# Optimization experiments

Measured on AMD Instinct MI355X. Metric: run time of the kernel, lower is better.

The kernel has to match this reference:

```python
import jax, jax.numpy as jnp
import numpy as np

D_MODEL = 384
N_HEADS = 8
HEAD_DIM = D_MODEL // N_HEADS


def setup_inputs() -> dict:
    key = jax.random.key(0)
    ks = jax.random.split(key, 8)
    b, n = 2, 2048
    s = 0.02
    return {
        "x": jax.random.normal(ks[0], (b, n, D_MODEL), jnp.float32),
        "coords": jax.random.normal(ks[1], (b, n, 3), jnp.float32),
        "W_qkv": jax.random.normal(ks[2], (D_MODEL, 3 * D_MODEL), jnp.float32) * s,
        "b_qkv": jnp.zeros((3 * D_MODEL,), jnp.float32),
        "W_dist": jax.random.normal(ks[3], (1, N_HEADS), jnp.float32) * s,
        "b_dist": jnp.zeros((N_HEADS,), jnp.float32),
        "W_out": jax.random.normal(ks[4], (D_MODEL, D_MODEL), jnp.float32) * s,
        "b_out": jnp.zeros((D_MODEL,), jnp.float32),
    }


def reference(x, coords, W_qkv, b_qkv, W_dist, b_dist, W_out, b_out):
    b, n, _ = x.shape
    qkv = x @ W_qkv + b_qkv                       # (b, n, 3*d)
    q, k, v = jnp.split(qkv, 3, axis=-1)
    def heads(t):
        return t.reshape(b, n, N_HEADS, HEAD_DIM).transpose(0, 2, 1, 3)  # b h n d
    q, k, v = heads(q), heads(k), heads(v)
    attn = jnp.einsum('bhid,bhjd->bhij', q, k) / jnp.sqrt(jnp.float32(HEAD_DIM))
    # distance bias: ||c_i - c_j|| projected to heads (Linear(1, n_heads))
    diff = coords[:, :, None, :] - coords[:, None, :, :]   # (b, i, j, 3)
    dist = jnp.sqrt(jnp.sum(diff * diff, axis=-1))         # (b, i, j)
    dist_bias = dist[..., None] * W_dist[0] + b_dist       # (b, i, j, h)
    attn = attn + dist_bias.transpose(0, 3, 1, 2)          # (b, h, i, j)
    attn = jax.nn.softmax(attn, axis=-1)
    out = jnp.einsum('bhij,bhjd->bhid', attn, v)
    out = out.transpose(0, 2, 1, 3).reshape(b, n, D_MODEL)
    return out @ W_out + b_out
```

## Files before the change

### kernel.cpp

```cpp
#include <hip/hip_runtime.h>
#include <hip/hip_bf16.h>

#define NB 2
#define SEQ 2048
#define DM 384
#define NH 8
#define HD 48
#define QKVN 1152

typedef __hip_bfloat16 bf16;
typedef __attribute__((ext_vector_type(8))) short short8;
typedef __attribute__((ext_vector_type(4))) float float4v;
typedef __attribute__((ext_vector_type(16))) float f32x16;

static __device__ __forceinline__ float bf2f(bf16 v){ return __bfloat162float(v); }
static __device__ __forceinline__ float ldin(const void* p, size_t i, int isf){
    return isf ? ((const float*)p)[i] : bf2f(((const bf16*)p)[i]);
}
static __device__ __forceinline__ short f2b(float f){
    union { float f; unsigned u; } a; a.f = f;
    unsigned r = a.u + 0x7FFFu + ((a.u >> 16) & 1u);
    return (short)(r >> 16);
}
static __device__ __forceinline__ unsigned pk2(float a, float b){
    union { __hip_bfloat162 h; unsigned u; } r;
    r.h = __float22bfloat162_rn(float2{a, b});
    return r.u;
}
static __device__ __forceinline__ float bflo(unsigned u){
    union { unsigned u; float f; } a; a.u = u << 16; return a.f;
}
static __device__ __forceinline__ float bfhi(unsigned u){
    union { unsigned u; float f; } a; a.u = u & 0xFFFF0000u; return a.f;
}
static __device__ __forceinline__ short8 u4pack(unsigned w0, unsigned w1, unsigned w2, unsigned w3){
    union { unsigned u[4]; short8 s; } r; r.u[0]=w0; r.u[1]=w1; r.u[2]=w2; r.u[3]=w3; return r.s;
}
static __device__ __forceinline__ int detect_isf(const void* x){
    const unsigned short* xb = (const unsigned short*)x;
    int l = threadIdx.x & 63;
    union { unsigned u; float f; } a; a.u = ((unsigned)xb[2*l]) << 16;
    float ab = fabsf(a.f);
    int good = (a.f == 0.0f) || (ab > 9.765625e-4f && ab < 1024.0f);
    unsigned long long m = __ballot(good);
    return (__popcll(m) >= 32) ? 0 : 1;
}

__global__ __launch_bounds__(256) void k_wt(const void* __restrict__ x,
    const void* __restrict__ Wqkv, const void* __restrict__ Wout,
    const void* __restrict__ bqkv, const void* __restrict__ bout,
    const void* __restrict__ Wdist, const void* __restrict__ bdist,
    short* __restrict__ WqT, short* __restrict__ WoT,
    float* __restrict__ bqf, float* __restrict__ bof,
    float* __restrict__ wdf, float* __restrict__ bdf)
{
    const int isf = detect_isf(x);
    const int t = threadIdx.x;
    const int b = blockIdx.x;
    if (b < 576) {
        int bb, NW; const void* W; short* WT;
        if (b < 432) { bb = b;       NW = QKVN; W = Wqkv; WT = WqT; }
        else         { bb = b - 432; NW = DM;   W = Wout; WT = WoT; }
        int ntiles = NW >> 5;
        int kt = bb / ntiles, nt = bb % ntiles;
        int k0 = kt*32, n0 = nt*32;
        __shared__ float Ls[32][33];
        for (int idx = t; idx < 1024; idx += 256) {
            int r = idx >> 5, c = idx & 31;
            Ls[r][c] = ldin(W, (size_t)(k0+r)*NW + n0 + c, isf);
        }
        __syncthreads();
        for (int idx = t; idx < 1024; idx += 256) {
            int r2 = idx >> 5, c2 = idx & 31;
            WT[(size_t)(n0+r2)*DM + k0 + c2] = f2b(Ls[c2][r2]);
        }
    } else {
        int idx = (b - 576)*256 + t;
        const float log2e = 1.4426950408889634f;
        if (idx < QKVN) bqf[idx] = ldin(bqkv, idx, isf);
        else if (idx < QKVN + DM) bof[idx - QKVN] = ldin(bout, idx - QKVN, isf);
        else if (idx < QKVN + DM + NH) wdf[idx - QKVN - DM] = ldin(Wdist, idx - QKVN - DM, isf)*log2e;
        else if (idx < QKVN + DM + 2*NH) bdf[idx - QKVN - DM - NH] = ldin(bdist, idx - QKVN - DM - NH, isf)*log2e;
    }
}

__global__ __launch_bounds__(256) void k_qkv_dist(const void* __restrict__ x,
    const void* __restrict__ coords,
    const short* __restrict__ WT, const float* __restrict__ bias,
    short* __restrict__ qg3, short* __restrict__ kg3, short* __restrict__ vg3,
    short* __restrict__ dist8)
{
    __shared__ __align__(16) short As[64*72];
    __shared__ __align__(16) short Bs[128*72];
    __shared__ float cjx[16], cjy[16], cjz[16];
    const int isf = detect_isf(x);
    const int t = threadIdx.x;
    if (blockIdx.x >= 576) {
        const int b = blockIdx.x - 576;
        const int bb = b >> 8;
        const int jg = (b >> 1) & 127;
        const int j0 = jg * 16;
        const int ih = (b & 1) * 1024;
        if (t < 16) {
            int gj = (bb*SEQ + j0 + t)*3;
            cjx[t] = ldin(coords, gj, isf);
            cjy[t] = ldin(coords, gj+1, isf);
            cjz[t] = ldin(coords, gj+2, isf);
        }
        __syncthreads();
        #pragma unroll
        for (int k = 0; k < 4; ++k) {
            int i = ih + k*256 + t;
            int gi = (bb*SEQ + i)*3;
            float px = ldin(coords, gi, isf), py = ldin(coords, gi+1, isf), pz = ldin(coords, gi+2, isf);
            short o[16];
            #pragma unroll
            for (int e = 0; e < 16; ++e) {
                float dx = px - cjx[e], dy = py - cjy[e], dz = pz - cjz[e];
                o[e] = f2b(sqrtf(dx*dx + dy*dy + dz*dz));
            }
            short* dst = dist8 + (((size_t)bb*512 + (size_t)jg*4)*SEQ + i)*4;
            *(int2*)(dst)          = *(const int2*)(o);
            *(int2*)(dst + SEQ*4)  = *(const int2*)(o + 4);
            *(int2*)(dst + SEQ*8)  = *(const int2*)(o + 8);
            *(int2*)(dst + SEQ*12) = *(const int2*)(o + 12);
        }
        return;
    }
    const int w = t >> 6, lane = t & 63, L = lane & 15, quad = lane >> 4;
    const int mt = blockIdx.x / 9, nt = blockIdx.x % 9;
    const int row0 = mt*64, col0 = nt*128;
    const int wm = w & 1, wn = w >> 1;
    float4v acc[2][4] = {};
    for (int k0 = 0; k0 < DM; k0 += 64) {
        __syncthreads();
        for (int c = t; c < 512; c += 256) {
            int row = c >> 3, k8 = c & 7;
            size_t src = (size_t)(row0+row)*DM + k0 + k8*8;
            if (isf) {
                const float* xf = (const float*)x + src;
                short o[8];
                #pragma unroll
                for (int e = 0; e < 8; ++e) o[e] = f2b(xf[e]);
                *(int4*)(&As[row*72 + k8*8]) = *(const int4*)o;
            } else {
                *(int4*)(&As[row*72 + k8*8]) = *(const int4*)((const short*)x + src);
            }
        }
        for (int c = t; c < 1024; c += 256) {
            int row = c >> 3, k8 = c & 7;
            *(int4*)(&Bs[row*72 + k8*8]) = *(const int4*)(WT + (size_t)(col0+row)*DM + k0 + k8*8);
        }
        __syncthreads();
        #pragma unroll
        for (int kc = 0; kc < 2; ++kc) {
            short8 a0 = *(const short8*)(&As[(32*wm + L)*72 + kc*32 + quad*8]);
            short8 a1 = *(const short8*)(&As[(32*wm + 16 + L)*72 + kc*32 + quad*8]);
            #pragma unroll
            for (int ni = 0; ni < 4; ++ni) {
                short8 bf = *(const short8*)(&Bs[(64*wn + 16*ni + L)*72 + kc*32 + quad*8]);
                acc[0][ni] = __builtin_amdgcn_mfma_f32_16x16x32_bf16(a0, bf, acc[0][ni], 0, 0, 0);
                acc[1][ni] = __builtin_amdgcn_mfma_f32_16x16x32_bf16(a1, bf, acc[1][ni], 0, 0, 0);
            }
        }
    }
    const int which = col0 / DM;
    const int cbase = col0 % DM;
    short* Ep = Bs;
    __syncthreads();
    if (which < 2) {
        #pragma unroll
        for (int mi = 0; mi < 2; ++mi)
            #pragma unroll
            for (int ni = 0; ni < 4; ++ni) {
                int col_l = 64*wn + 16*ni + L;
                float bv = bias[col0 + col_l];
                #pragma unroll
                for (int r = 0; r < 4; ++r) {
                    int row_l = 32*wm + 16*mi + quad*4 + r;
                    Ep[row_l*136 + col_l] = f2b(acc[mi][ni][r] + bv);
                }
            }
        __syncthreads();
        short* dst = which ? kg3 : qg3;
        for (int c = t; c < 1024; c += 256) {
            int row_l = c >> 4, col_l = (c & 15)*8;
            int row_g = row0 + row_l;
            int bi = row_g >> 11, nn = row_g & (SEQ-1);
            int c2 = cbase + col_l;
            int hh = c2/HD, dh = c2%HD;
            int bh = bi*NH + hh;
            int dc = dh >> 4, hi = (dh >> 3) & 1;
            size_t dstoff = ((size_t)bh*64 + (nn>>5))*1536 + (size_t)((dc*2 + hi)*256 + (nn&31)*8);
            *(int4*)(dst + dstoff) = *(const int4*)(&Ep[row_l*136 + col_l]);
        }
    } else {
        #pragma unroll
        for (int mi = 0; mi < 2; ++mi)
            #pragma unroll
            for (int ni = 0; ni < 4; ++ni) {
                int col_l = 64*wn + 16*ni + L;
                float bv = bias[col0 + col_l];
                #pragma unroll
                for (int r = 0; r < 4; ++r) {
                    int row_l = 32*wm + 16*mi + quad*4 + r;
                    Ep[col_l*72 + row_l] = f2b(acc[mi][ni][r] + bv);
                }
            }
        __syncthreads();
        for (int c = t; c < 1024; c += 256) {
            int col_l = c >> 3, row8 = (c & 7)*8;
            int row_g = row0 + row8;
            int bi = row_g >> 11, nn = row_g & (SEQ-1);
            int c2 = cbase + col_l;
            int hh = c2/HD, dh = c2%HD;
            int bh = bi*NH + hh;
            int jt = nn >> 5, jc = (nn >> 4) & 1;
            int ehalf = ((nn >> 3) & 1)*4;
            int dt = dh >> 5, dp = dh & 31;
            int hstride = dt ? 128 : 256;
            size_t base = ((size_t)bh*64 + jt)*1536 + (size_t)(jc*768 + dt*512 + dp*8 + ehalf);
            *(int2*)(vg3 + base)           = *(const int2*)(&Ep[col_l*72 + row8]);
            *(int2*)(vg3 + base + hstride) = *(const int2*)(&Ep[col_l*72 + row8 + 4]);
        }
    }
}

__global__ __launch_bounds__(256, 4) void k_attn(
    const short* __restrict__ qg3, const short* __restrict__ kg3, const short* __restrict__ vg3,
    const short* __restrict__ dist8, const float* __restrict__ wdf,
    const float* __restrict__ bdf, short* __restrict__ aob)
{
    __shared__ float Ored[2][32*48];
    __shared__ float Lred[2][32];
    const int t = threadIdx.x;
    const int w = t >> 6, lane = t & 63;
    const int li = lane & 31, hi = lane >> 5;
    const int xcd  = blockIdx.x & 7;
    const int slot = blockIdx.x >> 3;
    const int bi   = xcd >> 2;
    const int band = xcd & 3;
    const int hh   = slot & 7;
    const int it   = band*16 + (slot >> 3);
    const int bh   = bi*NH + hh;
    const int i0 = it*32;
    const float scale2 = 0.14433756729740643f * 1.4426950408889634f;
    const float wd = wdf[hh], bd = bdf[hh];

    const short* qB = qg3 + ((size_t)bh*64 + it)*1536 + hi*256 + li*8;
    const short8 qf0 = *(const short8*)(qB);
    const short8 qf1 = *(const short8*)(qB + 512);
    const short8 qf2 = *(const short8*)(qB + 1024);

    f32x16 accO0 = {}, accO1 = {};
    float rsum = 0.0f;

    const short* kBp = kg3 + ((size_t)bh*64 + w)*1536 + hi*256 + li*8;
    const short* vBp = vg3 + ((size_t)bh*64 + w)*1536 + li*8;
    const short* dBp = dist8 + (((size_t)bi*512 + (size_t)w*8 + hi)*SEQ + i0 + li)*4;

    for (int s = 0; s < 16; ++s) {
        short8 kf0 = *(const short8*)(kBp);
        short8 kf1 = *(const short8*)(kBp + 512);
        short8 kf2 = *(const short8*)(kBp + 1024);
        int2 du0 = *(const int2*)(dBp);
        int2 du1 = *(const int2*)(dBp + SEQ*8);
        int2 du2 = *(const int2*)(dBp + SEQ*16);
        int2 du3 = *(const int2*)(dBp + SEQ*24);
        f32x16 sacc = {};
        __builtin_amdgcn_s_setprio(1);
        sacc = __builtin_amdgcn_mfma_f32_32x32x16_bf16(kf0, qf0, sacc, 0, 0, 0);
        sacc = __builtin_amdgcn_mfma_f32_32x32x16_bf16(kf1, qf1, sacc, 0, 0, 0);
        sacc = __builtin_amdgcn_mfma_f32_32x32x16_bf16(kf2, qf2, sacc, 0, 0, 0);
        __builtin_amdgcn_s_setprio(0);
        float p[16];
        #pragma unroll
        for (int rq = 0; rq < 4; ++rq) {
            int2 du = rq == 0 ? du0 : rq == 1 ? du1 : rq == 2 ? du2 : du3;
            float d0 = bflo((unsigned)du.x), d1 = bfhi((unsigned)du.x);
            float d2 = bflo((unsigned)du.y), d3 = bfhi((unsigned)du.y);
            p[4*rq+0] = __builtin_amdgcn_exp2f(fmaf(sacc[4*rq+0], scale2, fmaf(d0, wd, bd)));
            p[4*rq+1] = __builtin_amdgcn_exp2f(fmaf(sacc[4*rq+1], scale2, fmaf(d1, wd, bd)));
            p[4*rq+2] = __builtin_amdgcn_exp2f(fmaf(sacc[4*rq+2], scale2, fmaf(d2, wd, bd)));
            p[4*rq+3] = __builtin_amdgcn_exp2f(fmaf(sacc[4*rq+3], scale2, fmaf(d3, wd, bd)));
            rsum += (p[4*rq+0] + p[4*rq+1]) + (p[4*rq+2] + p[4*rq+3]);
        }
        short8 pa0 = u4pack(pk2(p[0],p[1]),  pk2(p[2],p[3]),  pk2(p[4],p[5]),   pk2(p[6],p[7]));
        short8 pa1 = u4pack(pk2(p[8],p[9]),  pk2(p[10],p[11]),pk2(p[12],p[13]), pk2(p[14],p[15]));
        short8 v00 = *(const short8*)(vBp + hi*256);
        short8 v10 = *(const short8*)(vBp + 768 + hi*256);
        short8 v01 = *(const short8*)(vBp + 512 + hi*128);
        short8 v11 = *(const short8*)(vBp + 1280 + hi*128);
        __builtin_amdgcn_s_setprio(1);
        accO0 = __builtin_amdgcn_mfma_f32_32x32x16_bf16(pa0, v00, accO0, 0, 0, 0);
        accO0 = __builtin_amdgcn_mfma_f32_32x32x16_bf16(pa1, v10, accO0, 0, 0, 0);
        accO1 = __builtin_amdgcn_mfma_f32_32x32x16_bf16(pa0, v01, accO1, 0, 0, 0);
        accO1 = __builtin_amdgcn_mfma_f32_32x32x16_bf16(pa1, v11, accO1, 0, 0, 0);
        __builtin_amdgcn_s_setprio(0);
        kBp += 4*1536; vBp += 4*1536; dBp += (size_t)SEQ*128;
    }
    rsum += __shfl_xor(rsum, 32);

    if (w >= 2) {
        float* Od = Ored[w-2];
        #pragma unroll
        for (int r = 0; r < 16; ++r) {
            int ii = (r & 3) + 8*(r >> 2) + 4*hi;
            Od[ii*48 + li] = accO0[r];
            if (li < 16) Od[ii*48 + 32 + li] = accO1[r];
        }
        if (lane < 32) Lred[w-2][lane] = rsum;
    }
    __syncthreads();
    if (w < 2) {
        const float* Od = Ored[w];
        #pragma unroll
        for (int r = 0; r < 16; ++r) {
            int ii = (r & 3) + 8*(r >> 2) + 4*hi;
            accO0[r] += Od[ii*48 + li];
            accO1[r] += Od[ii*48 + 32 + (li & 15)];
        }
        rsum += Lred[w][li];
    }
    __syncthreads();
    if (w == 1) {
        float* Od = Ored[0];
        #pragma unroll
        for (int r = 0; r < 16; ++r) {
            int ii = (r & 3) + 8*(r >> 2) + 4*hi;
            Od[ii*48 + li] = accO0[r];
            if (li < 16) Od[ii*48 + 32 + li] = accO1[r];
        }
        if (lane < 32) Lred[0][lane] = rsum;
    }
    __syncthreads();
    if (w == 0) {
        float* Od = Ored[0];
        #pragma unroll
        for (int r = 0; r < 16; ++r) {
            int ii = (r & 3) + 8*(r >> 2) + 4*hi;
            Od[ii*48 + li] += accO0[r];
            if (li < 16) Od[ii*48 + 32 + li] += accO1[r];
        }
        if (lane < 32) Lred[0][lane] += rsum;
    }
    __syncthreads();
    for (int c = t; c < 192; c += 256) {
        int r = c / 6, d8 = (c % 6)*8;
        float inv = 1.0f / Lred[0][r];
        const float* src = &Ored[0][r*48 + d8];
        short o[8];
        #pragma unroll
        for (int e = 0; e < 8; ++e) o[e] = f2b(src[e]*inv);
        *(int4*)(aob + ((size_t)(bi*SEQ) + i0 + r)*DM + hh*HD + d8) = *(const int4*)o;
    }
}

__global__ __launch_bounds__(256) void k_out(const short* __restrict__ aob,
    const short* __restrict__ WT, const float* __restrict__ bias,
    void* __restrict__ out, const void* __restrict__ x)
{
    __shared__ __align__(16) short As[64*72];
    __shared__ __align__(16) short Bs[128*72];
    const int isf = detect_isf(x);
    const int t = threadIdx.x;
    const int w = t >> 6, lane = t & 63, L = lane & 15, quad = lane >> 4;
    const int mt = blockIdx.x / 3, nt = blockIdx.x % 3;
    const int row0 = mt*64, col0 = nt*128;
    const int wm = w & 1, wn = w >> 1;
    float4v acc[2][4] = {};
    for (int k0 = 0; k0 < DM; k0 += 64) {
        __syncthreads();
        for (int c = t; c < 512; c += 256) {
            int row = c >> 3, k8 = c & 7;
            *(int4*)(&As[row*72 + k8*8]) = *(const int4*)(aob + (size_t)(row0+row)*DM + k0 + k8*8);
        }
        for (int c = t; c < 1024; c += 256) {
            int row = c >> 3, k8 = c & 7;
            *(int4*)(&Bs[row*72 + k8*8]) = *(const int4*)(WT + (size_t)(col0+row)*DM + k0 + k8*8);
        }
        __syncthreads();
        #pragma unroll
        for (int kc = 0; kc < 2; ++kc) {
            short8 a0 = *(const short8*)(&As[(32*wm + L)*72 + kc*32 + quad*8]);
            short8 a1 = *(const short8*)(&As[(32*wm + 16 + L)*72 + kc*32 + quad*8]);
            #pragma unroll
            for (int ni = 0; ni < 4; ++ni) {
                short8 bf = *(const short8*)(&Bs[(64*wn + 16*ni + L)*72 + kc*32 + quad*8]);
                acc[0][ni] = __builtin_amdgcn_mfma_f32_16x16x32_bf16(a0, bf, acc[0][ni], 0, 0, 0);
                acc[1][ni] = __builtin_amdgcn_mfma_f32_16x16x32_bf16(a1, bf, acc[1][ni], 0, 0, 0);
            }
        }
    }
    #pragma unroll
    for (int mi = 0; mi < 2; ++mi) {
        #pragma unroll
        for (int ni = 0; ni < 4; ++ni) {
            int col_g = col0 + 64*wn + 16*ni + L;
            float bv = bias[col_g];
            #pragma unroll
            for (int r = 0; r < 4; ++r) {
                int row_g = row0 + 32*wm + 16*mi + quad*4 + r;
                size_t oi = (size_t)row_g*DM + col_g;
                float val = acc[mi][ni][r] + bv;
                if (isf) ((float*)out)[oi] = val;
                else     ((bf16*)out)[oi]  = __float2bfloat16(val);
            }
        }
    }
}

extern "C" void kernel_launch(void* const* d_in, const int* in_sizes, int n_in,
                              void* d_out, int out_size, void* d_ws, size_t ws_size,
                              hipStream_t stream) {
    const void* x      = d_in[0];
    const void* coords = d_in[1];
    const void* Wqkv   = d_in[2];
    const void* bqkv   = d_in[3];
    const void* Wdist  = d_in[4];
    const void* bdist  = d_in[5];
    const void* Wout   = d_in[6];
    const void* bout   = d_in[7];

    short* qg3   = (short*)d_ws;
    short* kg3   = qg3  + (size_t)1572864;
    short* vg3   = kg3  + (size_t)1572864;
    short* dist8 = vg3  + (size_t)1573120;
    short* aob   = dist8 + (size_t)8388608;
    short* WqT   = aob  + (size_t)1572864;
    short* WoT   = WqT  + (size_t)442368;
    float* bqf   = (float*)(WoT + (size_t)147456);
    float* bof   = bqf + QKVN;
    float* wdf   = bof + DM;
    float* bdf   = wdf + NH;

    k_wt<<<dim3(583), dim3(256), 0, stream>>>(x, Wqkv, Wout, bqkv, bout, Wdist, bdist,
                                              WqT, WoT, bqf, bof, wdf, bdf);
    k_qkv_dist<<<dim3(1088), dim3(256), 0, stream>>>(x, coords, WqT, bqf,
                                                     qg3, kg3, vg3, dist8);
    k_attn<<<dim3(1024), dim3(256), 0, stream>>>(qg3, kg3, vg3, dist8, wdf, bdf, aob);
    k_out<<<dim3(64*3), dim3(256), 0, stream>>>(aob, WoT, bof, d_out, x);
}
```

Before: 143.8 us.

## Register-prefetch GEMM tiles, move Wout transpose into QKV kernel, read biases directly

```diff
diff --git a/kernel.cpp b/kernel.cpp
--- a/kernel.cpp
+++ b/kernel.cpp
@@ -47,56 +47,56 @@
 }
 
 __global__ __launch_bounds__(256) void k_wt(const void* __restrict__ x,
-    const void* __restrict__ Wqkv, const void* __restrict__ Wout,
-    const void* __restrict__ bqkv, const void* __restrict__ bout,
-    const void* __restrict__ Wdist, const void* __restrict__ bdist,
-    short* __restrict__ WqT, short* __restrict__ WoT,
-    float* __restrict__ bqf, float* __restrict__ bof,
-    float* __restrict__ wdf, float* __restrict__ bdf)
+    const void* __restrict__ Wqkv, short* __restrict__ WqT)
 {
     const int isf = detect_isf(x);
     const int t = threadIdx.x;
     const int b = blockIdx.x;
-    if (b < 576) {
-        int bb, NW; const void* W; short* WT;
-        if (b < 432) { bb = b;       NW = QKVN; W = Wqkv; WT = WqT; }
-        else         { bb = b - 432; NW = DM;   W = Wout; WT = WoT; }
-        int ntiles = NW >> 5;
-        int kt = bb / ntiles, nt = bb % ntiles;
-        int k0 = kt*32, n0 = nt*32;
-        __shared__ float Ls[32][33];
-        for (int idx = t; idx < 1024; idx += 256) {
-            int r = idx >> 5, c = idx & 31;
-            Ls[r][c] = ldin(W, (size_t)(k0+r)*NW + n0 + c, isf);
-        }
-        __syncthreads();
-        for (int idx = t; idx < 1024; idx += 256) {
-            int r2 = idx >> 5, c2 = idx & 31;
-            WT[(size_t)(n0+r2)*DM + k0 + c2] = f2b(Ls[c2][r2]);
-        }
-    } else {
-        int idx = (b - 576)*256 + t;
-        const float log2e = 1.4426950408889634f;
-        if (idx < QKVN) bqf[idx] = ldin(bqkv, idx, isf);
-        else if (idx < QKVN + DM) bof[idx - QKVN] = ldin(bout, idx - QKVN, isf);
-        else if (idx < QKVN + DM + NH) wdf[idx - QKVN - DM] = ldin(Wdist, idx - QKVN - DM, isf)*log2e;
-        else if (idx < QKVN + DM + 2*NH) bdf[idx - QKVN - DM - NH] = ldin(bdist, idx - QKVN - DM - NH, isf)*log2e;
+    const int kt = b / 36, nt = b % 36;
+    const int k0 = kt*32, n0 = nt*32;
+    __shared__ float Ls[32][33];
+    for (int idx = t; idx < 1024; idx += 256) {
+        int r = idx >> 5, c = idx & 31;
+        Ls[r][c] = ldin(Wqkv, (size_t)(k0+r)*QKVN + n0 + c, isf);
+    }
+    __syncthreads();
+    for (int idx = t; idx < 1024; idx += 256) {
+        int r2 = idx >> 5, c2 = idx & 31;
+        WqT[(size_t)(n0+r2)*DM + k0 + c2] = f2b(Ls[c2][r2]);
     }
 }
 
 __global__ __launch_bounds__(256) void k_qkv_dist(const void* __restrict__ x,
     const void* __restrict__ coords,
-    const short* __restrict__ WT, const float* __restrict__ bias,
+    const short* __restrict__ WT, const void* __restrict__ bqkv,
+    const void* __restrict__ Wout,
     short* __restrict__ qg3, short* __restrict__ kg3, short* __restrict__ vg3,
-    short* __restrict__ dist8)
+    short* __restrict__ dist8, short* __restrict__ WoT)
 {
     __shared__ __align__(16) short As[64*72];
     __shared__ __align__(16) short Bs[128*72];
     __shared__ float cjx[16], cjy[16], cjz[16];
     const int isf = detect_isf(x);
     const int t = threadIdx.x;
-    if (blockIdx.x >= 576) {
-        const int b = blockIdx.x - 576;
+    const int bid = blockIdx.x;
+    if (bid >= 1088) {
+        const int b = bid - 1088;
+        const int kt = b / 12, nt = b % 12;
+        const int k0 = kt*32, n0 = nt*32;
+        float (*Ls)[33] = (float(*)[33])As;
+        for (int idx = t; idx < 1024; idx += 256) {
+            int r = idx >> 5, c = idx & 31;
+            Ls[r][c] = ldin(Wout, (size_t)(k0+r)*DM + n0 + c, isf);
+        }
+        __syncthreads();
+        for (int idx = t; idx < 1024; idx += 256) {
+            int r2 = idx >> 5, c2 = idx & 31;
+            WoT[(size_t)(n0+r2)*DM + k0 + c2] = f2b(Ls[c2][r2]);
+        }
+        return;
+    }
+    if (bid >= 576) {
+        const int b = bid - 576;
         const int bb = b >> 8;
         const int jg = (b >> 1) & 127;
         const int j0 = jg * 16;
@@ -128,30 +128,70 @@
         return;
     }
     const int w = t >> 6, lane = t & 63, L = lane & 15, quad = lane >> 4;
-    const int mt = blockIdx.x / 9, nt = blockIdx.x % 9;
+    const int mt = bid / 9, nt = bid % 9;
     const int row0 = mt*64, col0 = nt*128;
     const int wm = w & 1, wn = w >> 1;
     float4v acc[2][4] = {};
-    for (int k0 = 0; k0 < DM; k0 += 64) {
-        __syncthreads();
-        for (int c = t; c < 512; c += 256) {
-            int row = c >> 3, k8 = c & 7;
+    int4 rA[4], rB[4];
+    {
+        const int k0 = 0;
+        #pragma unroll
+        for (int ci = 0; ci < 2; ++ci) {
+            int c = t + ci*256; int row = c >> 3, k8 = c & 7;
             size_t src = (size_t)(row0+row)*DM + k0 + k8*8;
             if (isf) {
-                const float* xf = (const float*)x + src;
+                rA[2*ci]   = *(const int4*)((const float*)x + src);
+                rA[2*ci+1] = *(const int4*)((const float*)x + src + 4);
+            } else {
+                rA[ci] = *(const int4*)((const short*)x + src);
+            }
+        }
+        #pragma unroll
+        for (int ci = 0; ci < 4; ++ci) {
+            int c = t + ci*256; int row = c >> 3, k8 = c & 7;
+            rB[ci] = *(const int4*)(WT + (size_t)(col0+row)*DM + k0 + k8*8);
+        }
+    }
+    for (int ks = 0; ks < 6; ++ks) {
+        __syncthreads();
+        #pragma unroll
+        for (int ci = 0; ci < 2; ++ci) {
+            int c = t + ci*256; int row = c >> 3, k8 = c & 7;
+            if (isf) {
+                union { int4 i[2]; float f[8]; } u; u.i[0] = rA[2*ci]; u.i[1] = rA[2*ci+1];
                 short o[8];
                 #pragma unroll
-                for (int e = 0; e < 8; ++e) o[e] = f2b(xf[e]);
+                for (int e = 0; e < 8; ++e) o[e] = f2b(u.f[e]);
                 *(int4*)(&As[row*72 + k8*8]) = *(const int4*)o;
             } else {
-                *(int4*)(&As[row*72 + k8*8]) = *(const int4*)((const short*)x + src);
-            }
-        }
-        for (int c = t; c < 1024; c += 256) {
-            int row = c >> 3, k8 = c & 7;
-            *(int4*)(&Bs[row*72 + k8*8]) = *(const int4*)(WT + (size_t)(col0+row)*DM + k0 + k8*8);
-        }
-        __syncthreads();
+                *(int4*)(&As[row*72 + k8*8]) = rA[ci];
+            }
+        }
+        #pragma unroll
+        for (int ci = 0; ci < 4; ++ci) {
+            int c = t + ci*256; int row = c >> 3, k8 = c & 7;
+            *(int4*)(&Bs[row*72 + k8*8]) = rB[ci];
+        }
+        __syncthreads();
+        if (ks < 5) {
+            const int k0 = (ks+1)*64;
+            #pragma unroll
+            for (int ci = 0; ci < 2; ++ci) {
+                int c = t + ci*256; int row = c >> 3, k8 = c & 7;
+                size_t src = (size_t)(row0+row)*DM + k0 + k8*8;
+                if (isf) {
+                    rA[2*ci]   = *(const int4*)((const float*)x + src);
+                    rA[2*ci+1] = *(const int4*)((const float*)x + src + 4);
+                } else {
+                    rA[ci] = *(const int4*)((const short*)x + src);
+                }
+            }
+            #pragma unroll
+            for (int ci = 0; ci < 4; ++ci) {
+                int c = t + ci*256; int row = c >> 3, k8 = c & 7;
+                rB[ci] = *(const int4*)(WT + (size_t)(col0+row)*DM + k0 + k8*8);
+            }
+        }
         #pragma unroll
         for (int kc = 0; kc < 2; ++kc) {
             short8 a0 = *(const short8*)(&As[(32*wm + L)*72 + kc*32 + quad*8]);
@@ -174,7 +214,7 @@
             #pragma unroll
             for (int ni = 0; ni < 4; ++ni) {
                 int col_l = 64*wn + 16*ni + L;
-                float bv = bias[col0 + col_l];
+                float bv = ldin(bqkv, col0 + col_l, isf);
                 #pragma unroll
                 for (int r = 0; r < 4; ++r) {
                     int row_l = 32*wm + 16*mi + quad*4 + r;
@@ -200,7 +240,7 @@
             #pragma unroll
             for (int ni = 0; ni < 4; ++ni) {
                 int col_l = 64*wn + 16*ni + L;
-                float bv = bias[col0 + col_l];
+                float bv = ldin(bqkv, col0 + col_l, isf);
                 #pragma unroll
                 for (int r = 0; r < 4; ++r) {
                     int row_l = 32*wm + 16*mi + quad*4 + r;
@@ -228,11 +268,12 @@
 
 __global__ __launch_bounds__(256, 4) void k_attn(
     const short* __restrict__ qg3, const short* __restrict__ kg3, const short* __restrict__ vg3,
-    const short* __restrict__ dist8, const float* __restrict__ wdf,
-    const float* __restrict__ bdf, short* __restrict__ aob)
+    const short* __restrict__ dist8, const void* __restrict__ Wdist,
+    const void* __restrict__ bdist, short* __restrict__ aob, const void* __restrict__ x)
 {
     __shared__ float Ored[2][32*48];
     __shared__ float Lred[2][32];
+    const int isf = detect_isf(x);
     const int t = threadIdx.x;
     const int w = t >> 6, lane = t & 63;
     const int li = lane & 31, hi = lane >> 5;
@@ -244,8 +285,10 @@
     const int it   = band*16 + (slot >> 3);
     const int bh   = bi*NH + hh;
     const int i0 = it*32;
-    const float scale2 = 0.14433756729740643f * 1.4426950408889634f;
-    const float wd = wdf[hh], bd = bdf[hh];
+    const float log2e = 1.4426950408889634f;
+    const float scale2 = 0.14433756729740643f * log2e;
+    const float wd = ldin(Wdist, hh, isf) * log2e;
+    const float bd = ldin(bdist, hh, isf) * log2e;
 
     const short* qB = qg3 + ((size_t)bh*64 + it)*1536 + hi*256 + li*8;
     const short8 qf0 = *(const short8*)(qB);
@@ -357,7 +400,7 @@
 }
 
 __global__ __launch_bounds__(256) void k_out(const short* __restrict__ aob,
-    const short* __restrict__ WT, const float* __restrict__ bias,
+    const short* __restrict__ WT, const void* __restrict__ bout,
     void* __restrict__ out, const void* __restrict__ x)
 {
     __shared__ __align__(16) short As[64*72];
@@ -369,17 +412,45 @@
     const int row0 = mt*64, col0 = nt*128;
     const int wm = w & 1, wn = w >> 1;
     float4v acc[2][4] = {};
-    for (int k0 = 0; k0 < DM; k0 += 64) {
-        __syncthreads();
-        for (int c = t; c < 512; c += 256) {
-            int row = c >> 3, k8 = c & 7;
-            *(int4*)(&As[row*72 + k8*8]) = *(const int4*)(aob + (size_t)(row0+row)*DM + k0 + k8*8);
-        }
-        for (int c = t; c < 1024; c += 256) {
-            int row = c >> 3, k8 = c & 7;
-            *(int4*)(&Bs[row*72 + k8*8]) = *(const int4*)(WT + (size_t)(col0+row)*DM + k0 + k8*8);
-        }
-        __syncthreads();
+    int4 rA[2], rB[4];
+    {
+        #pragma unroll
+        for (int ci = 0; ci < 2; ++ci) {
+            int c = t + ci*256; int row = c >> 3, k8 = c & 7;
+            rA[ci] = *(const int4*)(aob + (size_t)(row0+row)*DM + k8*8);
+        }
+        #pragma unroll
+        for (int ci = 0; ci < 4; ++ci) {
+            int c = t + ci*256; int row = c >> 3, k8 = c & 7;
+            rB[ci] = *(const int4*)(WT + (size_t)(col0+row)*DM + k8*8);
+        }
+    }
+    for (int ks = 0; ks < 6; ++ks) {
+        __syncthreads();
+        #pragma unroll
+        for (int ci = 0; ci < 2; ++ci) {
+            int c = t + ci*256; int row = c >> 3, k8 = c & 7;
+            *(int4*)(&As[row*72 + k8*8]) = rA[ci];
+        }
+        #pragma unroll
+        for (int ci = 0; ci < 4; ++ci) {
+            int c = t + ci*256; int row = c >> 3, k8 = c & 7;
+            *(int4*)(&Bs[row*72 + k8*8]) = rB[ci];
+        }
+        __syncthreads();
+        if (ks < 5) {
+            const int k0 = (ks+1)*64;
+            #pragma unroll
+            for (int ci = 0; ci < 2; ++ci) {
+                int c = t + ci*256; int row = c >> 3, k8 = c & 7;
+                rA[ci] = *(const int4*)(aob + (size_t)(row0+row)*DM + k0 + k8*8);
+            }
+            #pragma unroll
+            for (int ci = 0; ci < 4; ++ci) {
+                int c = t + ci*256; int row = c >> 3, k8 = c & 7;
+                rB[ci] = *(const int4*)(WT + (size_t)(col0+row)*DM + k0 + k8*8);
+            }
+        }
         #pragma unroll
         for (int kc = 0; kc < 2; ++kc) {
             short8 a0 = *(const short8*)(&As[(32*wm + L)*72 + kc*32 + quad*8]);
@@ -397,7 +468,7 @@
         #pragma unroll
         for (int ni = 0; ni < 4; ++ni) {
             int col_g = col0 + 64*wn + 16*ni + L;
-            float bv = bias[col_g];
+            float bv = ldin(bout, col_g, isf);
             #pragma unroll
             for (int r = 0; r < 4; ++r) {
                 int row_g = row0 + 32*wm + 16*mi + quad*4 + r;
@@ -429,15 +500,10 @@
     short* aob   = dist8 + (size_t)8388608;
     short* WqT   = aob  + (size_t)1572864;
     short* WoT   = WqT  + (size_t)442368;
-    float* bqf   = (float*)(WoT + (size_t)147456);
-    float* bof   = bqf + QKVN;
-    float* wdf   = bof + DM;
-    float* bdf   = wdf + NH;
-
-    k_wt<<<dim3(583), dim3(256), 0, stream>>>(x, Wqkv, Wout, bqkv, bout, Wdist, bdist,
-                                              WqT, WoT, bqf, bof, wdf, bdf);
-    k_qkv_dist<<<dim3(1088), dim3(256), 0, stream>>>(x, coords, WqT, bqf,
-                                                     qg3, kg3, vg3, dist8);
-    k_attn<<<dim3(1024), dim3(256), 0, stream>>>(qg3, kg3, vg3, dist8, wdf, bdf, aob);
-    k_out<<<dim3(64*3), dim3(256), 0, stream>>>(aob, WoT, bof, d_out, x);
-}
+
+    k_wt<<<dim3(432), dim3(256), 0, stream>>>(x, Wqkv, WqT);
+    k_qkv_dist<<<dim3(1232), dim3(256), 0, stream>>>(x, coords, WqT, bqkv, Wout,
+                                                     qg3, kg3, vg3, dist8, WoT);
+    k_attn<<<dim3(1024), dim3(256), 0, stream>>>(qg3, kg3, vg3, dist8, Wdist, bdist, aob, x);
+    k_out<<<dim3(192), dim3(256), 0, stream>>>(aob, WoT, bout, d_out, x);
+}
```

Result: slower. 160.5 us (+11.6%).
